# Performance work log

Hardware: AMD Instinct MI355X
Metric: run time of the kernel (lower is better)

The kernel has to match this reference:

```python
import jax, jax.numpy as jnp
import numpy as np

EMBED_DIM = 1024
NUM_HEADS = 16
HEAD_DIM = EMBED_DIM // NUM_HEADS
B, T = 4, 2048


def setup_inputs() -> dict:
    key = jax.random.key(0)
    ks = jax.random.split(key, 5)
    s = 0.02
    return {
        "x": jax.random.normal(ks[0], (B, T, EMBED_DIM), dtype=jnp.float32),
        "W_qkv": jax.random.normal(ks[1], (EMBED_DIM, 3 * EMBED_DIM), dtype=jnp.float32) * s,
        "b_qkv": jnp.zeros((3 * EMBED_DIM,), dtype=jnp.float32),
        "W_proj": jax.random.normal(ks[2], (EMBED_DIM, EMBED_DIM), dtype=jnp.float32) * s,
        "b_proj": jnp.zeros((EMBED_DIM,), dtype=jnp.float32),
    }


def reference(x, W_qkv, b_qkv, W_proj, b_proj):
    # Dropout disabled (eval mode) for deterministic reference.
    Bsz, Tlen, C = x.shape
    qkv = x @ W_qkv + b_qkv                          # [B,T,3C]
    q, k, v = jnp.split(qkv, 3, axis=-1)
    def heads(t):  # [B,T,C] -> [B,H,T,Dh]
        return t.reshape(Bsz, Tlen, NUM_HEADS, HEAD_DIM).transpose(0, 2, 1, 3)
    q, k, v = heads(q), heads(k), heads(v)
    scale = HEAD_DIM ** -0.5
    wei = jnp.einsum("bhqd,bhkd->bhqk", q, k) * scale  # [B,H,T,T]
    causal = jnp.tril(jnp.ones((Tlen, Tlen), dtype=bool))
    wei = jnp.where(causal[None, None], wei, -jnp.inf)
    wei = jax.nn.softmax(wei, axis=-1)
    out = jnp.einsum("bhqk,bhkd->bhqd", wei, v)        # [B,H,T,Dh]
    out = out.transpose(0, 2, 1, 3).reshape(Bsz, Tlen, C)
    return out @ W_proj + b_proj
```

## Files before the change

### kernel.cpp

```cpp
#include <hip/hip_runtime.h>

#define DEV __device__ __forceinline__

using u16 = unsigned short;
using u32 = unsigned int;
typedef __attribute__((ext_vector_type(8)))  short  short8;
typedef __attribute__((ext_vector_type(8)))  u16    ushort8;
typedef __attribute__((ext_vector_type(4)))  u16    us4;
typedef __attribute__((ext_vector_type(4)))  float  f32x4;
typedef __attribute__((ext_vector_type(16))) float  f32x16;

constexpr int BB = 4;
constexpr int TT = 2048;
constexpr int CC = 1024;
constexpr int HH = 16;
constexpr int DD = 64;
constexpr int MM = BB * TT;
constexpr int N1 = 3 * CC;

DEV u16 f2bf(float f) {
    unsigned u = __float_as_uint(f);
    unsigned r = (u + 0x7FFFu + ((u >> 16) & 1u)) >> 16;
    return (u16)r;
}

DEV u32 cvtpk(float lo, float hi) {
    u32 r;
    asm("v_cvt_pk_bf16_f32 %0, %1, %2" : "=v"(r) : "v"(lo), "v"(hi));
    return r;
}

DEV void gload_lds16(const void* g, void* l) {
    __builtin_amdgcn_global_load_lds((const __attribute__((address_space(1))) void*)g,
                                     (__attribute__((address_space(3))) void*)l,
                                     16, 0, 0);
}

__global__ void k_cvt_x(const float* __restrict__ src, u16* __restrict__ dst) {
    int i = (blockIdx.x * 256 + threadIdx.x) * 8;
    f32x4 a = *(const f32x4*)(src + i);
    f32x4 b = *(const f32x4*)(src + i + 4);
    ushort8 u;
    u[0] = f2bf(a[0]); u[1] = f2bf(a[1]); u[2] = f2bf(a[2]); u[3] = f2bf(a[3]);
    u[4] = f2bf(b[0]); u[5] = f2bf(b[1]); u[6] = f2bf(b[2]); u[7] = f2bf(b[3]);
    *(ushort8*)(dst + i) = u;
}

__global__ __launch_bounds__(256) void k_transpose_cvt2(const float* __restrict__ src,
                                                        u16* __restrict__ dst,
                                                        int Kd, int Nd) {
    __shared__ u16 tile[64][66];
    const int t = threadIdx.x;
    const int k0 = blockIdx.y * 64, n0 = blockIdx.x * 64;
    const int c = t & 63, r0 = (t >> 6) * 16;
#pragma unroll
    for (int i = 0; i < 16; ++i)
        tile[r0 + i][c] = f2bf(src[(size_t)(k0 + r0 + i) * Nd + n0 + c]);
    __syncthreads();
    const int kc = (t & 7) * 8, nn = t >> 3;
#pragma unroll
    for (int h = 0; h < 2; ++h) {
        int n = nn + h * 32;
        ushort8 v;
#pragma unroll
        for (int j = 0; j < 8; ++j) v[j] = tile[kc + j][n];
        *(ushort8*)(dst + (size_t)(n0 + n) * Kd + k0 + kc) = v;
    }
}

DEV void stage_tile(const u16* __restrict__ Ag, const u16* __restrict__ Bg, int kt,
                    u16* As, u16* Bs, int lane, int wid) {
#pragma unroll
    for (int p = 0; p < 2; ++p) {
        int cb = p * 256 + wid * 64;
        int chunk = cb + lane;
        int row = chunk >> 2, kc = chunk & 3;
        gload_lds16(Ag + (size_t)row * 1024 + kt + kc * 8, As + cb * 8);
        gload_lds16(Bg + (size_t)row * 1024 + kt + kc * 8, Bs + cb * 8);
    }
}

DEV void gemm_mainloop2(const u16* __restrict__ Ag, const u16* __restrict__ Bg,
                        u16 (*As)[4096], u16 (*Bs)[4096], f32x4 acc[4][4]) {
    const int tid = threadIdx.x, lane = tid & 63, wid = tid >> 6;
    const int wr = wid >> 1, wc = wid & 1;
    stage_tile(Ag, Bg, 0, As[0], Bs[0], lane, wid);
    int cur = 0;
#pragma unroll 1
    for (int kt = 0; kt < 1024; kt += 32) {
        asm volatile("s_waitcnt vmcnt(0)" ::: "memory");
        __syncthreads();
        if (kt + 32 < 1024)
            stage_tile(Ag, Bg, kt + 32, As[cur ^ 1], Bs[cur ^ 1], lane, wid);
        short8 aF[4], bF[4];
#pragma unroll
        for (int m = 0; m < 4; ++m)
            aF[m] = *(const short8*)&As[cur][(wr * 64 + m * 16 + (lane & 15)) * 32 + (lane >> 4) * 8];
#pragma unroll
        for (int n = 0; n < 4; ++n)
            bF[n] = *(const short8*)&Bs[cur][(wc * 64 + n * 16 + (lane & 15)) * 32 + (lane >> 4) * 8];
        __builtin_amdgcn_s_setprio(1);
#pragma unroll
        for (int m = 0; m < 4; ++m)
#pragma unroll
            for (int n = 0; n < 4; ++n)
                acc[m][n] = __builtin_amdgcn_mfma_f32_16x16x32_bf16(aF[m], bF[n], acc[m][n], 0, 0, 0);
        __builtin_amdgcn_s_setprio(0);
        cur ^= 1;
    }
}

__global__ __launch_bounds__(256) void k_gemm_qkv(const u16* __restrict__ xb,
                                                  const u16* __restrict__ wt,
                                                  const float* __restrict__ bqkv,
                                                  u16* __restrict__ qb,
                                                  u16* __restrict__ kb,
                                                  u16* __restrict__ vtb) {
    __shared__ u16 As[2][4096], Bs[2][4096];
    f32x4 acc[4][4];
#pragma unroll
    for (int m = 0; m < 4; ++m)
#pragma unroll
        for (int n = 0; n < 4; ++n) acc[m][n] = (f32x4){0.f, 0.f, 0.f, 0.f};
    const int orig = blockIdx.y * 64 + blockIdx.x;
    const int swz = (orig & 7) * 192 + (orig >> 3);
    const int rowBase = (swz & 63) * 128, colBase = (swz >> 6) * 128;
    gemm_mainloop2(xb + (size_t)rowBase * 1024, wt + (size_t)colBase * 1024, As, Bs, acc);
    const int lane = threadIdx.x & 63, wid = threadIdx.x >> 6;
    const int wr = wid >> 1, wc = wid & 1;
#pragma unroll
    for (int n = 0; n < 4; ++n) {
        int gn = colBase + wc * 64 + n * 16 + (lane & 15);
        float bias = bqkv[gn];
        int which = gn >> 10, cc = gn & 1023, hh = cc >> 6, d = cc & 63;
        if (which == 2) {
            u16* vdst = vtb + ((size_t)hh * DD + d) * TT;
#pragma unroll
            for (int m = 0; m < 4; ++m) {
                int gm = rowBase + wr * 64 + m * 16 + (lane >> 4) * 4;
                int b = gm >> 11, t = gm & 2047;
                us4 pv;
#pragma unroll
                for (int r = 0; r < 4; ++r) pv[r] = f2bf(acc[m][n][r] + bias);
                *(us4*)(vdst + (size_t)b * (HH * DD * TT) + t) = pv;
            }
        } else {
            u16* dst = (which == 0 ? qb : kb);
            float sc = (which == 0) ? 0.125f : 1.0f;
#pragma unroll
            for (int m = 0; m < 4; ++m) {
#pragma unroll
                for (int r = 0; r < 4; ++r) {
                    int gm = rowBase + wr * 64 + m * 16 + (lane >> 4) * 4 + r;
                    int b = gm >> 11, t = gm & 2047;
                    dst[(((size_t)b * HH + hh) * TT + t) * DD + d] = f2bf((acc[m][n][r] + bias) * sc);
                }
            }
        }
    }
}

__global__ __launch_bounds__(256) void k_gemm_proj(const u16* __restrict__ ob,
                                                   const u16* __restrict__ wt,
                                                   const float* __restrict__ bproj,
                                                   float* __restrict__ out) {
    __shared__ u16 As[2][4096], Bs[2][4096];
    f32x4 acc[4][4];
#pragma unroll
    for (int m = 0; m < 4; ++m)
#pragma unroll
        for (int n = 0; n < 4; ++n) acc[m][n] = (f32x4){0.f, 0.f, 0.f, 0.f};
    const int orig = blockIdx.y * 64 + blockIdx.x;
    const int swz = (orig & 7) * 64 + (orig >> 3);
    const int rowBase = (swz & 63) * 128, colBase = (swz >> 6) * 128;
    gemm_mainloop2(ob + (size_t)rowBase * 1024, wt + (size_t)colBase * 1024, As, Bs, acc);
    const int lane = threadIdx.x & 63, wid = threadIdx.x >> 6;
    const int wr = wid >> 1, wc = wid & 1;
#pragma unroll
    for (int n = 0; n < 4; ++n) {
        int gn = colBase + wc * 64 + n * 16 + (lane & 15);
        float bias = bproj[gn];
#pragma unroll
        for (int m = 0; m < 4; ++m) {
#pragma unroll
            for (int r = 0; r < 4; ++r) {
                int gm = rowBase + wr * 64 + m * 16 + (lane >> 4) * 4 + r;
                out[(size_t)gm * 1024 + gn] = acc[m][n][r] + bias;
            }
        }
    }
}

__global__ __launch_bounds__(256) void k_attn2(const u16* __restrict__ qb,
                                               const u16* __restrict__ kb,
                                               const u16* __restrict__ vtb,
                                               u16* __restrict__ ob) {
    __shared__ u16 Kt[2][4096];
    __shared__ u16 Vs[2][4096];

    const int tid = threadIdx.x, lane = tid & 63, w = tid >> 6;
    const int h = lane >> 5, l31 = lane & 31;
    const int bh = blockIdx.x;
    const int qi = 15 - blockIdx.y;
    const size_t hb = (size_t)bh * (TT * DD);
    const int qw = qi * 128 + w * 32;
    const int nt_blk = 2 * qi + 2;
    const int nt_w = (qw >> 6) + 1;
    const int cb = tid & ~63;

    short8 qf[4];
#pragma unroll
    for (int df = 0; df < 4; ++df)
        qf[df] = *(const short8*)(qb + hb + (size_t)(qw + l31) * DD + df * 16 + h * 8);

    f32x16 o0, o1;
#pragma unroll
    for (int r = 0; r < 16; ++r) { o0[r] = 0.f; o1[r] = 0.f; }
    float mrun = -1e30f, lrun = 0.f;

#pragma unroll
    for (int part = 0; part < 2; ++part) {
        int c = part * 256 + tid;
        int row = c >> 3, sw = (c & 7) ^ (row & 7);
        gload_lds16(kb  + hb + (size_t)row * DD + sw * 8,      &Kt[0][(part * 256 + cb) * 8]);
        gload_lds16(vtb + hb + (size_t)row * TT + sw * 8,      &Vs[0][(part * 256 + cb) * 8]);
    }

    int cur = 0;
    for (int j = 0; j < nt_blk; ++j) {
        asm volatile("s_waitcnt vmcnt(0)" ::: "memory");
        __syncthreads();
        if (j + 1 < nt_blk) {
            const int jb = j + 1, nb = cur ^ 1;
#pragma unroll
            for (int part = 0; part < 2; ++part) {
                int c = part * 256 + tid;
                int row = c >> 3, sw = (c & 7) ^ (row & 7);
                gload_lds16(kb  + hb + (size_t)(jb * 64 + row) * DD + sw * 8, &Kt[nb][(part * 256 + cb) * 8]);
                gload_lds16(vtb + hb + (size_t)row * TT + jb * 64 + sw * 8,   &Vs[nb][(part * 256 + cb) * 8]);
            }
        }
        if (j < nt_w) {
            f32x16 s0, s1;
#pragma unroll
            for (int r = 0; r < 16; ++r) { s0[r] = 0.f; s1[r] = 0.f; }
            __builtin_amdgcn_s_setprio(1);
#pragma unroll
            for (int df = 0; df < 4; ++df) {
                int colsw = df * 2 + h;
                int sw = (colsw ^ (l31 & 7)) * 8;
                short8 k0 = *(const short8*)&Kt[cur][l31 * 64 + sw];
                short8 k1 = *(const short8*)&Kt[cur][(l31 + 32) * 64 + sw];
                s0 = __builtin_amdgcn_mfma_f32_32x32x16_bf16(k0, qf[df], s0, 0, 0, 0);
                s1 = __builtin_amdgcn_mfma_f32_32x32x16_bf16(k1, qf[df], s1, 0, 0, 0);
            }
            __builtin_amdgcn_s_setprio(0);

            if (j == nt_w - 1) {
                int qrel = qw + l31 - j * 64;
#pragma unroll
                for (int r = 0; r < 16; ++r) {
                    int kk = (r & 3) + 8 * (r >> 2) + 4 * h;
                    if (kk      > qrel) s0[r] = -1e30f;
                    if (kk + 32 > qrel) s1[r] = -1e30f;
                }
            }

            float pm = -1e30f;
#pragma unroll
            for (int r = 0; r < 16; ++r) pm = fmaxf(pm, fmaxf(s0[r], s1[r]));
            pm = fmaxf(pm, __shfl_xor(pm, 32));
            if (!__all(pm <= mrun + 8.f)) {
                float mnew = fmaxf(mrun, pm);
                float sc = __expf(mrun - mnew);
                mrun = mnew;
                lrun *= sc;
#pragma unroll
                for (int r = 0; r < 16; ++r) {
                    float scr = __shfl(sc, (r & 3) + 8 * (r >> 2) + 4 * h);
                    o0[r] *= scr; o1[r] *= scr;
                }
            }
            float sum = 0.f;
#pragma unroll
            for (int r = 0; r < 16; ++r) {
                float p0 = __expf(s0[r] - mrun); s0[r] = p0; sum += p0;
                float p1 = __expf(s1[r] - mrun); s1[r] = p1; sum += p1;
            }
            sum += __shfl_xor(sum, 32);
            lrun += sum;

            __builtin_amdgcn_s_setprio(1);
#pragma unroll
            for (int f = 0; f < 4; ++f) {
                const f32x16& P = (f >= 2) ? s1 : s0;
                u32 A0, A1, B0, B1;
                if (f & 1) { A0 = cvtpk(P[8],  P[9]);  A1 = cvtpk(P[10], P[11]);
                             B0 = cvtpk(P[12], P[13]); B1 = cvtpk(P[14], P[15]); }
                else       { A0 = cvtpk(P[0],  P[1]);  A1 = cvtpk(P[2],  P[3]);
                             B0 = cvtpk(P[4],  P[5]);  B1 = cvtpk(P[6],  P[7]);  }
                u32 U0 = h ? B0 : A0, U1 = h ? B1 : A1;
                u32 V0 = h ? A0 : B0, V1 = h ? A1 : B1;
                u32 W0 = (u32)__shfl_xor((int)V0, 32);
                u32 W1 = (u32)__shfl_xor((int)V1, 32);
                union { u32 u[4]; short8 s; } pa;
                pa.u[0] = h ? W0 : U0; pa.u[1] = h ? W1 : U1;
                pa.u[2] = h ? U0 : W0; pa.u[3] = h ? U1 : W1;
#pragma unroll
                for (int dt = 0; dt < 2; ++dt) {
                    int row = dt * 32 + l31;
                    short8 vf = *(const short8*)&Vs[cur][row * 64 + (((f * 2 + h) ^ (row & 7)) * 8)];
                    if (dt == 0) o0 = __builtin_amdgcn_mfma_f32_32x32x16_bf16(pa.s, vf, o0, 0, 0, 0);
                    else         o1 = __builtin_amdgcn_mfma_f32_32x32x16_bf16(pa.s, vf, o1, 0, 0, 0);
                }
            }
            __builtin_amdgcn_s_setprio(0);
        }
        cur ^= 1;
    }

    const int b = bh >> 4, head = bh & 15;
    float linv = 1.f / lrun;
#pragma unroll
    for (int r = 0; r < 16; ++r) {
        float li = __shfl(linv, (r & 3) + 8 * (r >> 2) + 4 * h);
        int q = qw + (r & 3) + 8 * (r >> 2) + 4 * h;
        size_t rb = ((size_t)(b * TT + q)) * CC + head * 64;
        ob[rb + l31]      = f2bf(o0[r] * li);
        ob[rb + 32 + l31] = f2bf(o1[r] * li);
    }
}

extern "C" void kernel_launch(void* const* d_in, const int* in_sizes, int n_in,
                              void* d_out, int out_size, void* d_ws, size_t ws_size,
                              hipStream_t stream) {
    const float* x     = (const float*)d_in[0];
    const float* Wqkv  = (const float*)d_in[1];
    const float* bqkv  = (const float*)d_in[2];
    const float* Wproj = (const float*)d_in[3];
    const float* bproj = (const float*)d_in[4];
    float* out = (float*)d_out;

    char* ws = (char*)d_ws;
    u16* xb    = (u16*)(ws + 0);
    u16* wqkvT = (u16*)(ws + 16777216);
    u16* wprojT= (u16*)(ws + 23068672);
    u16* qb    = (u16*)(ws + 25165824);
    u16* kb    = (u16*)(ws + 41943040);
    u16* vtb   = (u16*)(ws + 58720256);
    u16* ob    = xb;

    k_cvt_x<<<dim3(MM * CC / (256 * 8)), 256, 0, stream>>>(x, xb);
    k_transpose_cvt2<<<dim3(N1 / 64, CC / 64), 256, 0, stream>>>(Wqkv, wqkvT, CC, N1);
    k_transpose_cvt2<<<dim3(CC / 64, CC / 64), 256, 0, stream>>>(Wproj, wprojT, CC, CC);
    k_gemm_qkv<<<dim3(MM / 128, N1 / 128), 256, 0, stream>>>(xb, wqkvT, bqkv, qb, kb, vtb);
    k_attn2<<<dim3(BB * HH, TT / 128), 256, 0, stream>>>(qb, kb, vtb, ob);
    k_gemm_proj<<<dim3(MM / 128, CC / 128), 256, 0, stream>>>(ob, wprojT, bproj, out);
}
```

Measured before the change: 290.4 us.

## Triple-buffer GEMM and attention loads, widen attention blocks to 512 threads

Both GEMM mainloops and the attention kernel move from double to triple LDS buffering, prefetching two tiles ahead and waiting only on older loads (vmcnt(4)/vmcnt(2)) instead of draining all loads every iteration. The attention kernel now uses 512-thread blocks covering 256 query rows, so each staged K/V tile is shared by eight waves. The GEMM tile swizzle is removed in favour of plain block indexing. The aim is to hide global load latency and cut redundant K/V traffic, at the cost of more LDS per block, lower occupancy, and possibly worse L2 locality without the swizzle.

```diff
diff --git a/kernel.cpp b/kernel.cpp
--- a/kernel.cpp
+++ b/kernel.cpp
@@ -80,18 +80,22 @@
     }
 }
 
-DEV void gemm_mainloop2(const u16* __restrict__ Ag, const u16* __restrict__ Bg,
+DEV void gemm_mainloop3(const u16* __restrict__ Ag, const u16* __restrict__ Bg,
                         u16 (*As)[4096], u16 (*Bs)[4096], f32x4 acc[4][4]) {
     const int tid = threadIdx.x, lane = tid & 63, wid = tid >> 6;
     const int wr = wid >> 1, wc = wid & 1;
-    stage_tile(Ag, Bg, 0, As[0], Bs[0], lane, wid);
+    stage_tile(Ag, Bg, 0,  As[0], Bs[0], lane, wid);
+    stage_tile(Ag, Bg, 32, As[1], Bs[1], lane, wid);
     int cur = 0;
 #pragma unroll 1
-    for (int kt = 0; kt < 1024; kt += 32) {
-        asm volatile("s_waitcnt vmcnt(0)" ::: "memory");
-        __syncthreads();
-        if (kt + 32 < 1024)
-            stage_tile(Ag, Bg, kt + 32, As[cur ^ 1], Bs[cur ^ 1], lane, wid);
+    for (int t = 0; t < 32; ++t) {
+        if (t == 31) asm volatile("s_waitcnt vmcnt(0)" ::: "memory");
+        else         asm volatile("s_waitcnt vmcnt(4)" ::: "memory");
+        __builtin_amdgcn_s_barrier();
+        if (t + 2 < 32) {
+            int nb = cur + 2; if (nb > 2) nb -= 3;
+            stage_tile(Ag, Bg, (t + 2) * 32, As[nb], Bs[nb], lane, wid);
+        }
         short8 aF[4], bF[4];
 #pragma unroll
         for (int m = 0; m < 4; ++m)
@@ -106,7 +110,7 @@
             for (int n = 0; n < 4; ++n)
                 acc[m][n] = __builtin_amdgcn_mfma_f32_16x16x32_bf16(aF[m], bF[n], acc[m][n], 0, 0, 0);
         __builtin_amdgcn_s_setprio(0);
-        cur ^= 1;
+        cur = (cur == 2) ? 0 : cur + 1;
     }
 }
 
@@ -116,16 +120,14 @@
                                                   u16* __restrict__ qb,
                                                   u16* __restrict__ kb,
                                                   u16* __restrict__ vtb) {
-    __shared__ u16 As[2][4096], Bs[2][4096];
+    __shared__ u16 As[3][4096], Bs[3][4096];
     f32x4 acc[4][4];
 #pragma unroll
     for (int m = 0; m < 4; ++m)
 #pragma unroll
         for (int n = 0; n < 4; ++n) acc[m][n] = (f32x4){0.f, 0.f, 0.f, 0.f};
-    const int orig = blockIdx.y * 64 + blockIdx.x;
-    const int swz = (orig & 7) * 192 + (orig >> 3);
-    const int rowBase = (swz & 63) * 128, colBase = (swz >> 6) * 128;
-    gemm_mainloop2(xb + (size_t)rowBase * 1024, wt + (size_t)colBase * 1024, As, Bs, acc);
+    const int rowBase = blockIdx.x * 128, colBase = blockIdx.y * 128;
+    gemm_mainloop3(xb + (size_t)rowBase * 1024, wt + (size_t)colBase * 1024, As, Bs, acc);
     const int lane = threadIdx.x & 63, wid = threadIdx.x >> 6;
     const int wr = wid >> 1, wc = wid & 1;
 #pragma unroll
@@ -164,16 +166,14 @@
                                                    const u16* __restrict__ wt,
                                                    const float* __restrict__ bproj,
                                                    float* __restrict__ out) {
-    __shared__ u16 As[2][4096], Bs[2][4096];
+    __shared__ u16 As[3][4096], Bs[3][4096];
     f32x4 acc[4][4];
 #pragma unroll
     for (int m = 0; m < 4; ++m)
 #pragma unroll
         for (int n = 0; n < 4; ++n) acc[m][n] = (f32x4){0.f, 0.f, 0.f, 0.f};
-    const int orig = blockIdx.y * 64 + blockIdx.x;
-    const int swz = (orig & 7) * 64 + (orig >> 3);
-    const int rowBase = (swz & 63) * 128, colBase = (swz >> 6) * 128;
-    gemm_mainloop2(ob + (size_t)rowBase * 1024, wt + (size_t)colBase * 1024, As, Bs, acc);
+    const int rowBase = blockIdx.x * 128, colBase = blockIdx.y * 128;
+    gemm_mainloop3(ob + (size_t)rowBase * 1024, wt + (size_t)colBase * 1024, As, Bs, acc);
     const int lane = threadIdx.x & 63, wid = threadIdx.x >> 6;
     const int wr = wid >> 1, wc = wid & 1;
 #pragma unroll
@@ -191,22 +191,31 @@
     }
 }
 
-__global__ __launch_bounds__(256) void k_attn2(const u16* __restrict__ qb,
+DEV void attn_stage(const u16* __restrict__ kb_hb, const u16* __restrict__ vtb_hb,
+                    int j, u16* Kd, u16* Vd, int tid) {
+    int row = tid >> 3, sw = (tid & 7) ^ (row & 7);
+    int cb8 = (tid & ~63) * 8;
+    gload_lds16(kb_hb + (size_t)(j * 64 + row) * DD + sw * 8, Kd + cb8);
+    gload_lds16(vtb_hb + (size_t)row * TT + j * 64 + sw * 8,  Vd + cb8);
+}
+
+__global__ __launch_bounds__(512) void k_attn2(const u16* __restrict__ qb,
                                                const u16* __restrict__ kb,
                                                const u16* __restrict__ vtb,
                                                u16* __restrict__ ob) {
-    __shared__ u16 Kt[2][4096];
-    __shared__ u16 Vs[2][4096];
+    __shared__ u16 Kt[3][4096];
+    __shared__ u16 Vs[3][4096];
 
     const int tid = threadIdx.x, lane = tid & 63, w = tid >> 6;
     const int h = lane >> 5, l31 = lane & 31;
     const int bh = blockIdx.x;
-    const int qi = 15 - blockIdx.y;
+    const int qi = 7 - blockIdx.y;
     const size_t hb = (size_t)bh * (TT * DD);
-    const int qw = qi * 128 + w * 32;
-    const int nt_blk = 2 * qi + 2;
+    const int qw = qi * 256 + w * 32;
+    const int nt_blk = 4 * qi + 4;
     const int nt_w = (qw >> 6) + 1;
-    const int cb = tid & ~63;
+    const u16* kb_hb = kb + hb;
+    const u16* vtb_hb = vtb + hb;
 
     short8 qf[4];
 #pragma unroll
@@ -218,27 +227,17 @@
     for (int r = 0; r < 16; ++r) { o0[r] = 0.f; o1[r] = 0.f; }
     float mrun = -1e30f, lrun = 0.f;
 
-#pragma unroll
-    for (int part = 0; part < 2; ++part) {
-        int c = part * 256 + tid;
-        int row = c >> 3, sw = (c & 7) ^ (row & 7);
-        gload_lds16(kb  + hb + (size_t)row * DD + sw * 8,      &Kt[0][(part * 256 + cb) * 8]);
-        gload_lds16(vtb + hb + (size_t)row * TT + sw * 8,      &Vs[0][(part * 256 + cb) * 8]);
-    }
+    attn_stage(kb_hb, vtb_hb, 0, Kt[0], Vs[0], tid);
+    attn_stage(kb_hb, vtb_hb, 1, Kt[1], Vs[1], tid);
 
     int cur = 0;
     for (int j = 0; j < nt_blk; ++j) {
-        asm volatile("s_waitcnt vmcnt(0)" ::: "memory");
-        __syncthreads();
-        if (j + 1 < nt_blk) {
-            const int jb = j + 1, nb = cur ^ 1;
-#pragma unroll
-            for (int part = 0; part < 2; ++part) {
-                int c = part * 256 + tid;
-                int row = c >> 3, sw = (c & 7) ^ (row & 7);
-                gload_lds16(kb  + hb + (size_t)(jb * 64 + row) * DD + sw * 8, &Kt[nb][(part * 256 + cb) * 8]);
-                gload_lds16(vtb + hb + (size_t)row * TT + jb * 64 + sw * 8,   &Vs[nb][(part * 256 + cb) * 8]);
-            }
+        if (j == nt_blk - 1) asm volatile("s_waitcnt vmcnt(0)" ::: "memory");
+        else                 asm volatile("s_waitcnt vmcnt(2)" ::: "memory");
+        __builtin_amdgcn_s_barrier();
+        if (j + 2 < nt_blk) {
+            int nb = cur + 2; if (nb > 2) nb -= 3;
+            attn_stage(kb_hb, vtb_hb, j + 2, Kt[nb], Vs[nb], tid);
         }
         if (j < nt_w) {
             f32x16 s0, s1;
@@ -316,7 +315,7 @@
             }
             __builtin_amdgcn_s_setprio(0);
         }
-        cur ^= 1;
+        cur = (cur == 2) ? 0 : cur + 1;
     }
 
     const int b = bh >> 4, head = bh & 15;
@@ -354,6 +353,6 @@
     k_transpose_cvt2<<<dim3(N1 / 64, CC / 64), 256, 0, stream>>>(Wqkv, wqkvT, CC, N1);
     k_transpose_cvt2<<<dim3(CC / 64, CC / 64), 256, 0, stream>>>(Wproj, wprojT, CC, CC);
     k_gemm_qkv<<<dim3(MM / 128, N1 / 128), 256, 0, stream>>>(xb, wqkvT, bqkv, qb, kb, vtb);
-    k_attn2<<<dim3(BB * HH, TT / 128), 256, 0, stream>>>(qb, kb, vtb, ob);
+    k_attn2<<<dim3(BB * HH, TT / 256), 512, 0, stream>>>(qb, kb, vtb, ob);
     k_gemm_proj<<<dim3(MM / 128, CC / 128), 256, 0, stream>>>(ob, wprojT, bproj, out);
 }
```

Result: faster. 270.4 us (-6.9%).
